# Optimization experiments

Measured on AMD Instinct MI355X. Metric: run time of the kernel, lower is better.

The kernel has to match this reference:

```python
import jax, jax.numpy as jnp
import numpy as np
from jax import lax

CONF_T = 0.5
IOU_T = 0.5
STRIDE = 8.0
NA = 3            # anchors per cell
NO = 16           # x,y,w,h,obj,10 landmarks,cls
G = 80            # grid size for 640/8
K = 300           # max detections kept into NMS
ANCHORS = np.array([[4., 5.], [8., 10.], [13., 16.]], dtype=np.float32)


def _conv(x, w, b, stride):
    y = lax.conv_general_dilated(x, w, (stride, stride), 'SAME',
                                 dimension_numbers=('NCHW', 'OIHW', 'NCHW'))
    return jax.nn.silu(y + b[None, :, None, None])


def _nms_single(boxes, scores):
    # boxes [N,4] xyxy, scores [N] (0 where below conf threshold)
    top_scores, idx = lax.top_k(scores, K)
    b = boxes[idx]                                   # [K,4]
    x1, y1, x2, y2 = b[:, 0], b[:, 1], b[:, 2], b[:, 3]
    area = jnp.maximum(x2 - x1, 0.) * jnp.maximum(y2 - y1, 0.)
    ix1 = jnp.maximum(x1[:, None], x1[None, :])
    iy1 = jnp.maximum(y1[:, None], y1[None, :])
    ix2 = jnp.minimum(x2[:, None], x2[None, :])
    iy2 = jnp.minimum(y2[:, None], y2[None, :])
    inter = jnp.maximum(ix2 - ix1, 0.) * jnp.maximum(iy2 - iy1, 0.)
    iou = inter / (area[:, None] + area[None, :] - inter + 1e-7)   # [K,K]

    ar = jnp.arange(K)

    def body(i, keep):
        sup = keep[i] & (iou[i] > IOU_T) & (ar > i)
        return keep & ~sup

    keep = lax.fori_loop(0, K, body, jnp.ones((K,), bool))
    keep = keep & (top_scores > 0.)
    return jnp.concatenate(
        [b, top_scores[:, None], keep.astype(b.dtype)[:, None]], axis=-1)  # [K,6]


def setup_inputs() -> dict:
    key = jax.random.key(0)
    ks = jax.random.split(key, 9)
    s = 0.1
    return {
        'x':  jax.random.uniform(ks[0], (16, 3, 640, 640), jnp.float32),
        'W1': jax.random.normal(ks[1], (16, 3, 3, 3), jnp.float32) * s,
        'b1': jnp.zeros((16,), jnp.float32),
        'W2': jax.random.normal(ks[2], (32, 16, 3, 3), jnp.float32) * s,
        'b2': jnp.zeros((32,), jnp.float32),
        'W3': jax.random.normal(ks[3], (64, 32, 3, 3), jnp.float32) * s,
        'b3': jnp.zeros((64,), jnp.float32),
        'Wh': jax.random.normal(ks[4], (NA * NO, 64, 1, 1), jnp.float32) * s,
        'bh': jnp.zeros((NA * NO,), jnp.float32),
    }


def reference(x, W1, b1, W2, b2, W3, b3, Wh, bh):
    B = x.shape[0]
    # backbone: stride-8 conv stem (YOLOv5n-like)
    f = _conv(x, W1, b1, 2)      # [B,16,320,320]
    f = _conv(f, W2, b2, 2)      # [B,32,160,160]
    f = _conv(f, W3, b3, 2)      # [B,64,80,80]
    h = lax.conv_general_dilated(f, Wh, (1, 1), 'SAME',
                                 dimension_numbers=('NCHW', 'OIHW', 'NCHW'))
    h = h + bh[None, :, None, None]                  # [B,NA*NO,G,G]
    p = h.reshape(B, NA, NO, G, G).transpose(0, 1, 3, 4, 2)  # [B,NA,G,G,NO]
    p = jax.nn.sigmoid(p)

    gy, gx = jnp.meshgrid(jnp.arange(G, dtype=jnp.float32),
                          jnp.arange(G, dtype=jnp.float32), indexing='ij')
    grid = jnp.stack([gx, gy], axis=-1)              # [G,G,2]
    anchors = jnp.asarray(ANCHORS)

    xy = (p[..., 0:2] * 2. - 0.5 + grid[None, None]) * STRIDE
    wh = (p[..., 2:4] * 2.) ** 2 * anchors[None, :, None, None, :]
    score = p[..., 4] * p[..., 15]                   # obj * cls

    boxes = jnp.concatenate([xy - wh / 2., xy + wh / 2.], axis=-1)
    boxes = boxes.reshape(B, -1, 4)                  # [B,N,4]
    score = score.reshape(B, -1)                     # [B,N]
    score = jnp.where(score > CONF_T, score, 0.)

    return jax.vmap(_nms_single)(boxes, score)       # [B,K,6]
```

## Files before the change

kernel.cpp:

```cpp
#include <hip/hip_runtime.h>
#include <math.h>

#define BATCH 16
#define GRID  80
#define NANCH 3
#define KTOP  300
#define NBOX  (NANCH*GRID*GRID)
#define SORT_CAP 8192

__device__ __forceinline__ float sigmoidf_(float x){ return 1.0f/(1.0f+expf(-x)); }

template<int CIN,int COUT,int C,int ICCH,int HIN,int HOUT,int TX,int TY,int MINW>
__global__ __launch_bounds__(256, MINW) void conv3x3s2_v7(
    const float* __restrict__ in, const float* __restrict__ w,
    const float* __restrict__ bias, float* __restrict__ out)
{
  constexpr int NTX = TX/4, NTY = TY/2, NSP = NTX*NTY, OCG = COUT/C;
  static_assert(NSP*OCG == 256, "bad thread layout");
  static_assert(C==4 || C==8, "C must be 4 or 8");
  constexpr int HR = 2*TY+1, HC = 2*TX+1;
  constexpr int NB4  = HC/4;
  constexpr int PADC = ((HC+3)/4)*4 + 4;
  constexpr int ILDSC = HR*PADC;
  constexpr int TBX = HOUT/TX, TBY = HOUT/TY;
  static_assert(TBX*TX == HOUT && TBY*TY == HOUT, "no masking");
  constexpr int NCH  = CIN/ICCH;
  constexpr int NH4  = ICCH*HR*NB4;
  constexpr int NH1  = ICCH*HR;
  constexpr int NWT  = ICCH*9*COUT;
  constexpr int NLD4 = (NH4+255)/256;
  constexpr int NLD1 = (NH1+255)/256;
  constexpr int NLDW = (NWT+255)/256;
  __shared__ float ilds[2][ICCH*ILDSC];
  __shared__ float wlds[2][NWT];

  const int t  = threadIdx.x;
  const int sx = t % NTX;
  const int sy = (t / NTX) % NTY;
  const int og = t / NSP;
  int blk = blockIdx.x;
  const int bx = blk % TBX; blk /= TBX;
  const int by = blk % TBY; blk /= TBY;
  const int b  = blk;

  const int ix0 = bx*2*TX, iy0 = by*2*TY;
  const int ylim = (iy0 + HR <= HIN) ? HR : (HIN - iy0);
  const bool tail_ok = (ix0 + NB4*4 < HIN);

  float4 hreg[NLD4];
  float  treg[NLD1];
  float  wreg[NLDW];

  auto load_regs = [&](int c0){
    #pragma unroll
    for (int l=0;l<NLD4;++l){
      int i = t + 256*l;
      float4 v = make_float4(0.f,0.f,0.f,0.f);
      if (i < NH4){
        int c = i/(HR*NB4), rm = i - c*(HR*NB4);
        int r = rm/NB4, m = rm - r*NB4;
        if (r < ylim)
          v = *(const float4*)(in + (size_t)(b*CIN + c0 + c)*HIN*HIN
                                  + (size_t)(iy0+r)*HIN + ix0 + 4*m);
      }
      hreg[l] = v;
    }
    #pragma unroll
    for (int l=0;l<NLD1;++l){
      int i = t + 256*l;
      float v = 0.f;
      if (i < NH1){
        int c = i/HR, r = i - c*HR;
        if (r < ylim && tail_ok)
          v = in[(size_t)(b*CIN + c0 + c)*HIN*HIN + (size_t)(iy0+r)*HIN + ix0 + NB4*4];
      }
      treg[l] = v;
    }
    #pragma unroll
    for (int l=0;l<NLDW;++l){
      int i = t + 256*l;
      float v = 0.f;
      if (i < NWT){
        int oc  = i % COUT;
        int k   = (i / COUT) % 9;
        int icl = i / (9*COUT);
        v = w[((size_t)oc*CIN + c0+icl)*9 + k];
      }
      wreg[l] = v;
    }
  };

  auto write_lds = [&](int bufi){
    #pragma unroll
    for (int l=0;l<NLD4;++l){
      int i = t + 256*l;
      if (i < NH4){
        int c = i/(HR*NB4), rm = i - c*(HR*NB4);
        int r = rm/NB4, m = rm - r*NB4;
        *(float4*)(&ilds[bufi][c*ILDSC + r*PADC + 4*((r>>2)&1) + 4*m]) = hreg[l];
      }
    }
    #pragma unroll
    for (int l=0;l<NLD1;++l){
      int i = t + 256*l;
      if (i < NH1){
        int c = i/HR, r = i - c*HR;
        ilds[bufi][c*ILDSC + r*PADC + 4*((r>>2)&1) + NB4*4] = treg[l];
      }
    }
    #pragma unroll
    for (int l=0;l<NLDW;++l){
      int i = t + 256*l;
      if (i < NWT) wlds[bufi][i] = wreg[l];
    }
  };

  float acc[C][2][4];
  #pragma unroll
  for (int j=0;j<C;++j){
    float bv = bias[og*C+j];
    #pragma unroll
    for (int py=0;py<2;++py)
      #pragma unroll
      for (int px=0;px<4;++px) acc[j][py][px]=bv;
  }

  load_regs(0);
  write_lds(0);
  __syncthreads();

  #pragma unroll 1
  for (int ch=0; ch<NCH; ++ch){
    const int cur = ch & 1;
    if (ch+1 < NCH) load_regs((ch+1)*ICCH);

    #pragma unroll 1
    for (int icl=0; icl<ICCH; ++icl){
      const float* wpb = &wlds[cur][icl*9*COUT] + og*C;
      float4 wk0[9], wk1[9];
      #pragma unroll
      for (int k=0;k<9;++k){
        wk0[k] = *(const float4*)(wpb + k*COUT);
        if constexpr (C==8) wk1[k] = *(const float4*)(wpb + k*COUT + 4);
      }
      const float* ipb = &ilds[cur][icl*ILDSC] + 8*sx;
      float rw[5][12];
      #pragma unroll
      for (int r=0;r<5;++r){
        const int rr = 4*sy + r;
        const float* rp = ipb + rr*PADC + 4*((rr>>2)&1);
        #pragma unroll
        for (int m=0;m<3;++m){
          float4 v4 = *(const float4*)(rp + 4*m);
          rw[r][4*m+0]=v4.x; rw[r][4*m+1]=v4.y; rw[r][4*m+2]=v4.z; rw[r][4*m+3]=v4.w;
        }
      }
      #pragma unroll
      for (int py=0;py<2;++py)
        #pragma unroll
        for (int ky=0;ky<3;++ky)
          #pragma unroll
          for (int kx=0;kx<3;++kx){
            const float4 wa = wk0[ky*3+kx];
            #pragma unroll
            for (int px=0;px<4;++px){
              const float xv = rw[2*py+ky][2*px+kx];
              acc[0][py][px] += xv*wa.x; acc[1][py][px] += xv*wa.y;
              acc[2][py][px] += xv*wa.z; acc[3][py][px] += xv*wa.w;
            }
            if constexpr (C==8){
              const float4 wb = wk1[ky*3+kx];
              #pragma unroll
              for (int px=0;px<4;++px){
                const float xv = rw[2*py+ky][2*px+kx];
                acc[4][py][px] += xv*wb.x; acc[5][py][px] += xv*wb.y;
                acc[6][py][px] += xv*wb.z; acc[7][py][px] += xv*wb.w;
              }
            }
          }
    }

    if (ch+1 < NCH) write_lds((ch+1)&1);
    __syncthreads();
  }

  const int oxb = bx*TX + sx*4;
  #pragma unroll
  for (int j=0;j<C;++j){
    int oc = og*C+j;
    #pragma unroll
    for (int py=0;py<2;++py){
      int oy = by*TY + sy*2 + py;
      float4 o4;
      float z0=acc[j][py][0], z1=acc[j][py][1], z2=acc[j][py][2], z3=acc[j][py][3];
      o4.x = z0/(1.0f+expf(-z0));
      o4.y = z1/(1.0f+expf(-z1));
      o4.z = z2/(1.0f+expf(-z2));
      o4.w = z3/(1.0f+expf(-z3));
      *(float4*)(out + ((size_t)(b*COUT+oc)*HOUT + oy)*HOUT + oxb) = o4;
    }
  }
}

__global__ __launch_bounds__(256, 1) void conv2_v12(
    const float* __restrict__ in, const float* __restrict__ w,
    const float* __restrict__ bias, float* __restrict__ out)
{
  constexpr int CIN=16, COUT=32, HIN=320, HOUT=160, TX=32, TY=16;
  constexpr int NTX=8, NTY=8;
  constexpr int C=8;
  constexpr int HR=2*TY+1;
  constexpr int NB4=(2*TX+1)/4;
  constexpr int PADC=72;
  constexpr int ILDSC=HR*PADC;
  constexpr int TBX=HOUT/TX, TBY=HOUT/TY;
  constexpr int NH4=HR*NB4;
  constexpr int NH1=HR;
  constexpr int NLD4=(NH4+255)/256;
  __shared__ float ilds[2][ILDSC];

  const int t  = threadIdx.x;
  const int sx = t % NTX;
  const int sy = (t / NTX) % NTY;
  const int og = t / 64;
  const int ocb = __builtin_amdgcn_readfirstlane(og * C);

  int blk = blockIdx.x;
  const int bx = blk % TBX; blk /= TBX;
  const int by = blk % TBY; blk /= TBY;
  const int b  = blk;

  const int ix0 = bx*2*TX, iy0 = by*2*TY;
  const int ylim = (iy0 + HR <= HIN) ? HR : (HIN - iy0);
  const bool tail_ok = (ix0 + NB4*4 < HIN);

  float4 hreg[NLD4];
  float  treg;

  auto load_regs = [&](int c0){
    #pragma unroll
    for (int l=0;l<NLD4;++l){
      int i = t + 256*l;
      float4 v = make_float4(0.f,0.f,0.f,0.f);
      if (i < NH4){
        int r = i/NB4, m = i - r*NB4;
        if (r < ylim)
          v = *(const float4*)(in + (size_t)(b*CIN + c0)*HIN*HIN
                                  + (size_t)(iy0+r)*HIN + ix0 + 4*m);
      }
      hreg[l] = v;
    }
    {
      float v = 0.f;
      if (t < NH1){
        int r = t;
        if (r < ylim && tail_ok)
          v = in[(size_t)(b*CIN + c0)*HIN*HIN + (size_t)(iy0+r)*HIN + ix0 + NB4*4];
      }
      treg = v;
    }
  };

  auto write_lds = [&](int bufi){
    #pragma unroll
    for (int l=0;l<NLD4;++l){
      int i = t + 256*l;
      if (i < NH4){
        int r = i/NB4, m = i - r*NB4;
        *(float4*)(&ilds[bufi][r*PADC + 4*((r>>2)&1) + 4*m]) = hreg[l];
      }
    }
    if (t < NH1){
      int r = t;
      ilds[bufi][r*PADC + 4*((r>>2)&1) + NB4*4] = treg;
    }
  };

  float acc[C][2][4];
  #pragma unroll
  for (int j=0;j<C;++j){
    float bv = bias[og*C+j];
    #pragma unroll
    for (int py=0;py<2;++py)
      #pragma unroll
      for (int px=0;px<4;++px) acc[j][py][px]=bv;
  }

  load_regs(0);
  write_lds(0);
  __syncthreads();

  #pragma unroll 1
  for (int ch=0; ch<CIN; ++ch){
    const int cur = ch & 1;
    if (ch+1 < CIN) load_regs(ch+1);

    const float* wg = w + ((size_t)ocb*CIN + ch)*9;
    const float* ipb = &ilds[cur][0] + 8*sx;

    #pragma unroll
    for (int ky=0;ky<3;++ky){
      float wv[3][8];
      #pragma unroll
      for (int j=0;j<8;++j){
        #pragma unroll
        for (int kx=0;kx<3;++kx)
          wv[kx][j] = wg[(size_t)j*(CIN*9) + ky*3 + kx];
      }
      {
        float ra[12];
        const int rr0 = 4*sy + ky;
        const float* rp0 = ipb + rr0*PADC + 4*((rr0>>2)&1);
        #pragma unroll
        for (int m=0;m<3;++m){
          float4 v0 = *(const float4*)(rp0 + 4*m);
          ra[4*m+0]=v0.x; ra[4*m+1]=v0.y; ra[4*m+2]=v0.z; ra[4*m+3]=v0.w;
        }
        #pragma unroll
        for (int kx=0;kx<3;++kx){
          #pragma unroll
          for (int px=0;px<4;++px){
            const float xv = ra[2*px+kx];
            acc[0][0][px] += xv*wv[kx][0]; acc[1][0][px] += xv*wv[kx][1];
            acc[2][0][px] += xv*wv[kx][2]; acc[3][0][px] += xv*wv[kx][3];
            acc[4][0][px] += xv*wv[kx][4]; acc[5][0][px] += xv*wv[kx][5];
            acc[6][0][px] += xv*wv[kx][6]; acc[7][0][px] += xv*wv[kx][7];
          }
        }
      }
      {
        float rb[12];
        const int rr1 = 4*sy + ky + 2;
        const float* rp1 = ipb + rr1*PADC + 4*((rr1>>2)&1);
        #pragma unroll
        for (int m=0;m<3;++m){
          float4 v1 = *(const float4*)(rp1 + 4*m);
          rb[4*m+0]=v1.x; rb[4*m+1]=v1.y; rb[4*m+2]=v1.z; rb[4*m+3]=v1.w;
        }
        #pragma unroll
        for (int kx=0;kx<3;++kx){
          #pragma unroll
          for (int px=0;px<4;++px){
            const float xv = rb[2*px+kx];
            acc[0][1][px] += xv*wv[kx][0]; acc[1][1][px] += xv*wv[kx][1];
            acc[2][1][px] += xv*wv[kx][2]; acc[3][1][px] += xv*wv[kx][3];
            acc[4][1][px] += xv*wv[kx][4]; acc[5][1][px] += xv*wv[kx][5];
            acc[6][1][px] += xv*wv[kx][6]; acc[7][1][px] += xv*wv[kx][7];
          }
        }
      }
    }

    if (ch+1 < CIN) write_lds((ch+1)&1);
    __syncthreads();
  }

  const int oxb = bx*TX + sx*4;
  #pragma unroll
  for (int j=0;j<C;++j){
    int oc = og*C+j;
    #pragma unroll
    for (int py=0;py<2;++py){
      int oy = by*TY + sy*2 + py;
      float4 o4;
      float z0=acc[j][py][0], z1=acc[j][py][1], z2=acc[j][py][2], z3=acc[j][py][3];
      o4.x = z0/(1.0f+expf(-z0));
      o4.y = z1/(1.0f+expf(-z1));
      o4.z = z2/(1.0f+expf(-z2));
      o4.w = z3/(1.0f+expf(-z3));
      *(float4*)(out + ((size_t)(b*COUT+oc)*HOUT + oy)*HOUT + oxb) = o4;
    }
  }
}

__global__ __launch_bounds__(256, 1) void conv3_decode_fused(
    const float* __restrict__ in,
    const float* __restrict__ w,
    const float* __restrict__ bias,
    const float* __restrict__ wh,
    const float* __restrict__ bh,
    float* __restrict__ boxes, float* __restrict__ scores)
{
  constexpr int CIN=32, COUT=64, C=8, ICCH=4, HIN=160, TX=16, TY=8;
  constexpr int NTX=4, NTY=8;
  constexpr int HR=2*TY+1, HC=2*TX+1;
  constexpr int NB4=HC/4;
  constexpr int PADC=((HC+3)/4)*4+4;
  constexpr int ILDSC=HR*PADC;
  constexpr int TBX=5, TBY=10;
  constexpr int NCH=CIN/ICCH;
  constexpr int NH4=ICCH*HR*NB4;
  constexpr int NH1=ICCH*HR;
  constexpr int NWT=ICCH*9*COUT;
  constexpr int NLD4=(NH4+255)/256, NLD1=(NH1+255)/256, NLDW=(NWT+255)/256;
  constexpr int F3S=69;
  __shared__ float smem[10048];
  float* ildsb = smem;
  float* wldsb = smem + 5440;
  float* f3l   = smem;

  const int t  = threadIdx.x;
  const int sp = t & 31;
  const int sx = sp & 3;
  const int sy = sp >> 2;
  const int og = t >> 5;
  int blk = blockIdx.x;
  const int bx = blk % TBX; blk /= TBX;
  const int by = blk % TBY; blk /= TBY;
  const int b  = blk;

  const int ix0 = bx*2*TX, iy0 = by*2*TY;
  const int ylim = (iy0 + HR <= HIN) ? HR : (HIN - iy0);
  const bool tail_ok = (ix0 + NB4*4 < HIN);

  float4 hreg[NLD4];
  float  treg[NLD1];
  float  wreg[NLDW];

  auto load_regs = [&](int c0){
    #pragma unroll
    for (int l=0;l<NLD4;++l){
      int i = t + 256*l;
      float4 v = make_float4(0.f,0.f,0.f,0.f);
      if (i < NH4){
        int c = i/(HR*NB4), rm = i - c*(HR*NB4);
        int r = rm/NB4, m = rm - r*NB4;
        if (r < ylim)
          v = *(const float4*)(in + (size_t)(b*CIN + c0 + c)*HIN*HIN
                                  + (size_t)(iy0+r)*HIN + ix0 + 4*m);
      }
      hreg[l] = v;
    }
    #pragma unroll
    for (int l=0;l<NLD1;++l){
      int i = t + 256*l;
      float v = 0.f;
      if (i < NH1){
        int c = i/HR, r = i - c*HR;
        if (r < ylim && tail_ok)
          v = in[(size_t)(b*CIN + c0 + c)*HIN*HIN + (size_t)(iy0+r)*HIN + ix0 + NB4*4];
      }
      treg[l] = v;
    }
    #pragma unroll
    for (int l=0;l<NLDW;++l){
      int i = t + 256*l;
      float v = 0.f;
      if (i < NWT){
        int oc  = i % COUT;
        int k   = (i / COUT) % 9;
        int icl = i / (9*COUT);
        v = w[((size_t)oc*CIN + c0+icl)*9 + k];
      }
      wreg[l] = v;
    }
  };

  auto write_lds = [&](int bufi){
    #pragma unroll
    for (int l=0;l<NLD4;++l){
      int i = t + 256*l;
      if (i < NH4){
        int c = i/(HR*NB4), rm = i - c*(HR*NB4);
        int r = rm/NB4, m = rm - r*NB4;
        *(float4*)(&ildsb[bufi*(ICCH*ILDSC) + c*ILDSC + r*PADC + 4*((r>>2)&1) + 4*m]) = hreg[l];
      }
    }
    #pragma unroll
    for (int l=0;l<NLD1;++l){
      int i = t + 256*l;
      if (i < NH1){
        int c = i/HR, r = i - c*HR;
        ildsb[bufi*(ICCH*ILDSC) + c*ILDSC + r*PADC + 4*((r>>2)&1) + NB4*4] = treg[l];
      }
    }
    #pragma unroll
    for (int l=0;l<NLDW;++l){
      int i = t + 256*l;
      if (i < NWT) wldsb[bufi*NWT + i] = wreg[l];
    }
  };

  float acc[C][4];
  #pragma unroll
  for (int j=0;j<C;++j){
    float bv = bias[og*C+j];
    #pragma unroll
    for (int px=0;px<4;++px) acc[j][px]=bv;
  }

  load_regs(0);
  write_lds(0);
  __syncthreads();

  #pragma unroll 1
  for (int ch=0; ch<NCH; ++ch){
    const int cur = ch & 1;
    if (ch+1 < NCH) load_regs((ch+1)*ICCH);

    #pragma unroll 1
    for (int icl=0; icl<ICCH; ++icl){
      const float* wpb = &wldsb[cur*NWT + icl*9*COUT] + og*C;
      const float* ipb = &ildsb[cur*(ICCH*ILDSC) + icl*ILDSC] + 8*sx;
      #pragma unroll
      for (int ky=0;ky<3;++ky){
        float row[12];
        {
          const int rr = 2*sy + ky;
          const float* rp = ipb + rr*PADC + 4*((rr>>2)&1);
          #pragma unroll
          for (int m=0;m<3;++m){
            float4 v4 = *(const float4*)(rp + 4*m);
            row[4*m+0]=v4.x; row[4*m+1]=v4.y; row[4*m+2]=v4.z; row[4*m+3]=v4.w;
          }
        }
        #pragma unroll
        for (int kx=0;kx<3;++kx){
          const float4 wa = *(const float4*)(wpb + (ky*3+kx)*COUT);
          const float4 wb = *(const float4*)(wpb + (ky*3+kx)*COUT + 4);
          #pragma unroll
          for (int px=0;px<4;++px){
            const float xv = row[2*px+kx];
            acc[0][px] += xv*wa.x; acc[1][px] += xv*wa.y;
            acc[2][px] += xv*wa.z; acc[3][px] += xv*wa.w;
            acc[4][px] += xv*wb.x; acc[5][px] += xv*wb.y;
            acc[6][px] += xv*wb.z; acc[7][px] += xv*wb.w;
          }
        }
      }
    }

    if (ch+1 < NCH) write_lds((ch+1)&1);
    __syncthreads();
  }

  #pragma unroll
  for (int j=0;j<C;++j){
    int oc = og*C+j;
    #pragma unroll
    for (int px=0;px<4;++px){
      int pxidx = sy*16 + sx*4+px;
      float z = acc[j][px];
      f3l[pxidx*F3S + oc] = z/(1.0f+expf(-z));
    }
  }
  __syncthreads();

  const float awv[3] = {4.0f, 8.0f, 13.0f};
  const float ahv[3] = {5.0f, 10.0f, 16.0f};
  const int chs[6] = {0,1,2,3,4,15};
  for (int q=t; q<384; q+=256){
    int p = q & 127;
    const int ua = __builtin_amdgcn_readfirstlane(q >> 7);
    float ac[6];
    #pragma unroll
    for (int j=0;j<6;++j) ac[j] = bh[ua*16 + chs[j]];
    const float* fp = f3l + p*F3S;
    const float* wp = wh + (size_t)ua*16*64;
    #pragma unroll 4
    for (int ic=0; ic<64; ic+=4){
      float4 fv = *(const float4*)(fp + ic);
      #pragma unroll
      for (int j=0;j<6;++j){
        float4 wv = *(const float4*)(wp + chs[j]*64 + ic);
        ac[j] += fv.x*wv.x; ac[j] += fv.y*wv.y;
        ac[j] += fv.z*wv.z; ac[j] += fv.w*wv.w;
      }
    }
    float p0 = sigmoidf_(ac[0]);
    float p1 = sigmoidf_(ac[1]);
    float p2 = sigmoidf_(ac[2]);
    float p3 = sigmoidf_(ac[3]);
    float p4 = sigmoidf_(ac[4]);
    float p15= sigmoidf_(ac[5]);
    int gx = bx*16 + (p & 15), gy = by*8 + (p >> 4);
    float cx = (p0*2.0f - 0.5f + (float)gx)*8.0f;
    float cy = (p1*2.0f - 0.5f + (float)gy)*8.0f;
    float ww = p2*2.0f; ww = ww*ww*awv[ua];
    float hh = p3*2.0f; hh = hh*hh*ahv[ua];
    float sc = p4*p15;
    sc = (sc > 0.5f) ? sc : 0.0f;
    int bi = ua*GRID*GRID + gy*GRID + gx;
    float* bo = boxes + ((size_t)b*NBOX + bi)*4;
    bo[0] = cx - ww*0.5f;
    bo[1] = cy - hh*0.5f;
    bo[2] = cx + ww*0.5f;
    bo[3] = cy + hh*0.5f;
    scores[(size_t)b*NBOX + bi] = sc;
  }
}

__global__ __launch_bounds__(1024) void topk_kernel(
    const float* __restrict__ boxes, const float* __restrict__ scores,
    float* __restrict__ nmsbuf, int* __restrict__ mcnt)
{
  __shared__ unsigned long long keys[SORT_CAP];
  __shared__ int   cntM;
  __shared__ int   sel[KTOP];
  __shared__ float selsc[KTOP];
  __shared__ int   wsum[16];
  __shared__ float rs[16];
  __shared__ int   ri[16];
  __shared__ unsigned clm[(NBOX+31)/32];

  const int b = blockIdx.x;
  const int t = threadIdx.x;
  const int lane = t & 63, wv = t >> 6;
  const float* scp = scores + (size_t)b*NBOX;

  if (t == 0) cntM = 0;
  __syncthreads();

  for (int i=t; i<NBOX; i+=1024){
    float v = scp[i];
    if (v > 0.0f){
      int p = atomicAdd(&cntM, 1);
      if (p < SORT_CAP)
        keys[p] = ((unsigned long long)__float_as_uint(v) << 32)
                | (unsigned)(0xFFFFFFFFu - (unsigned)i);
    }
  }
  __syncthreads();
  const int M = cntM;
  if (t == 0) mcnt[b] = M;

  if (M <= SORT_CAP){
    int P = 64; while (P < M) P <<= 1;
    for (int i=t; i<P; i+=1024) if (i >= M) keys[i] = 0ULL;
    __syncthreads();
    for (int k=2; k<=P; k<<=1){
      for (int j=k>>1; j>0; j>>=1){
        for (int i=t; i<P; i+=1024){
          int ixj = i ^ j;
          if (ixj > i){
            unsigned long long a = keys[i], c = keys[ixj];
            bool up = ((i & k) == 0);
            if (up ? (a < c) : (a > c)){ keys[i] = c; keys[ixj] = a; }
          }
        }
        __syncthreads();
      }
    }
    const int top = (M < KTOP) ? M : KTOP;
    if (t < top){
      unsigned long long kk = keys[t];
      selsc[t] = __uint_as_float((unsigned)(kk >> 32));
      sel[t]   = (int)(0xFFFFFFFFu - (unsigned)(kk & 0xFFFFFFFFu));
    }
    if (M < KTOP){
      const int need = KTOP - M;
      const int Cc = (NBOX + 1023)/1024;
      int lo = t*Cc, hi = lo+Cc; if (hi > NBOX) hi = NBOX; if (lo > NBOX) lo = NBOX;
      int zc = 0;
      for (int i=lo;i<hi;i++) if (scp[i] <= 0.0f) zc++;
      int v = zc;
      #pragma unroll
      for (int off=1; off<64; off<<=1){
        int n = __shfl_up(v, off);
        if (lane >= off) v += n;
      }
      if (lane == 63) wsum[wv] = v;
      __syncthreads();
      if (t == 0){
        int a = 0;
        for (int w=0; w<16; w++){ int tmp = wsum[w]; wsum[w] = a; a += tmp; }
      }
      __syncthreads();
      int r = wsum[wv] + v - zc;
      for (int i=lo;i<hi;i++){
        if (scp[i] <= 0.0f){
          if (r < need){ sel[M+r] = i; selsc[M+r] = 0.0f; }
          r++;
        }
      }
    }
    __syncthreads();
  } else {
    for (int i=t; i<(NBOX+31)/32; i+=1024) clm[i] = 0u;
    __syncthreads();
    for (int k=0;k<KTOP;k++){
      float best = -2.0f; int bi = NBOX;
      for (int i=t;i<NBOX;i+=1024){
        if (!((clm[i>>5] >> (i&31)) & 1u)){
          float v = scp[i];
          if (v > best){ best=v; bi=i; }
        }
      }
      #pragma unroll
      for (int off=32; off>0; off>>=1){
        float ov = __shfl_down(best, off);
        int   oi = __shfl_down(bi,   off);
        if (ov > best || (ov == best && oi < bi)){ best=ov; bi=oi; }
      }
      if (lane == 0){ rs[wv]=best; ri[wv]=bi; }
      __syncthreads();
      if (t == 0){
        for (int w=1; w<16; w++)
          if (rs[w] > best || (rs[w] == best && ri[w] < bi)){ best=rs[w]; bi=ri[w]; }
        sel[k]=bi; selsc[k]=best; clm[bi>>5] |= (1u << (bi&31));
      }
      __syncthreads();
    }
  }

  if (t < KTOP){
    const float* bp = boxes + ((size_t)b*NBOX + sel[t])*4;
    float x1=bp[0], y1=bp[1], x2=bp[2], y2=bp[3];
    float* o = nmsbuf + ((size_t)b*KTOP + t)*6;
    o[0]=x1; o[1]=y1; o[2]=x2; o[3]=y2;
    o[4]=selsc[t];
    o[5]=fmaxf(x2-x1,0.0f)*fmaxf(y2-y1,0.0f);
  }
}

__global__ __launch_bounds__(64, 1) void nms_kernel(
    const float* __restrict__ nmsbuf, const int* __restrict__ mcnt,
    float* __restrict__ out)
{
  const int b = blockIdx.x;
  const int lane = threadIdx.x;
  int Mtop = mcnt[b]; if (Mtop > KTOP) Mtop = KTOP;
  float X1[5],Y1[5],X2[5],Y2[5],AR[5],SC[5];
  unsigned keepm = 0;
  #pragma unroll
  for (int s5=0; s5<5; ++s5){
    int j = lane + 64*s5;
    if (j < KTOP){
      const float* p = nmsbuf + ((size_t)b*KTOP + j)*6;
      X1[s5]=p[0]; Y1[s5]=p[1]; X2[s5]=p[2]; Y2[s5]=p[3];
      SC[s5]=p[4]; AR[s5]=p[5];
      keepm |= (1u << s5);
    } else { X1[s5]=0;Y1[s5]=0;X2[s5]=0;Y2[s5]=0;AR[s5]=0;SC[s5]=0; }
  }
  for (int i=0;i<Mtop;i++){
    const int iw = i & 63, is = i >> 6;
    unsigned km = __shfl(keepm, iw);
    if ((km >> is) & 1u){
      float sx1 = (is==0)?X1[0]:(is==1)?X1[1]:(is==2)?X1[2]:(is==3)?X1[3]:X1[4];
      float sy1 = (is==0)?Y1[0]:(is==1)?Y1[1]:(is==2)?Y1[2]:(is==3)?Y1[3]:Y1[4];
      float sx2 = (is==0)?X2[0]:(is==1)?X2[1]:(is==2)?X2[2]:(is==3)?X2[3]:X2[4];
      float sy2 = (is==0)?Y2[0]:(is==1)?Y2[1]:(is==2)?Y2[2]:(is==3)?Y2[3]:Y2[4];
      float sa  = (is==0)?AR[0]:(is==1)?AR[1]:(is==2)?AR[2]:(is==3)?AR[3]:AR[4];
      float bx1=__shfl(sx1,iw), by1=__shfl(sy1,iw);
      float bx2=__shfl(sx2,iw), by2=__shfl(sy2,iw);
      float ba =__shfl(sa ,iw);
      #pragma unroll
      for (int s5=0; s5<5; ++s5){
        int j = lane + 64*s5;
        if (((keepm >> s5) & 1u) && j > i){
          float ix1=fmaxf(bx1,X1[s5]);
          float iy1=fmaxf(by1,Y1[s5]);
          float ix2=fminf(bx2,X2[s5]);
          float iy2=fminf(by2,Y2[s5]);
          float inter=fmaxf(ix2-ix1,0.0f)*fmaxf(iy2-iy1,0.0f);
          float iou = inter/(ba+AR[s5]-inter+1e-7f);
          if (iou > 0.5f) keepm &= ~(1u << s5);
        }
      }
    }
  }
  #pragma unroll
  for (int s5=0; s5<5; ++s5){
    int j = lane + 64*s5;
    if (j < KTOP){
      float scv = SC[s5];
      float kf  = (((keepm >> s5) & 1u) && scv > 0.0f) ? 1.0f : 0.0f;
      float* o = out + ((size_t)b*KTOP + j)*6;
      o[0]=X1[s5]; o[1]=Y1[s5]; o[2]=X2[s5]; o[3]=Y2[s5];
      o[4]=scv; o[5]=kf;
    }
  }
}

extern "C" void kernel_launch(void* const* d_in, const int* in_sizes, int n_in,
                              void* d_out, int out_size, void* d_ws, size_t ws_size,
                              hipStream_t stream) {
  const float* x  = (const float*)d_in[0];
  const float* W1 = (const float*)d_in[1];
  const float* b1 = (const float*)d_in[2];
  const float* W2 = (const float*)d_in[3];
  const float* b2 = (const float*)d_in[4];
  const float* W3 = (const float*)d_in[5];
  const float* b3 = (const float*)d_in[6];
  const float* Wh = (const float*)d_in[7];
  const float* bh = (const float*)d_in[8];
  float* out = (float*)d_out;
  float* ws  = (float*)d_ws;

  float* f1     = ws;
  float* f2     = ws + 26214400;
  float* boxes  = ws;
  float* scores = boxes + 1228800;
  float* nmsbuf = scores + 307200;
  int*   mcnt   = (int*)(nmsbuf + 28800);

  conv3x3s2_v7<3,16,8,1,640,320,64,16,1><<<5*20*BATCH, 256, 0, stream>>>(x,  W1, b1, f1);
  conv2_v12<<<5*10*BATCH, 256, 0, stream>>>(f1, W2, b2, f2);
  conv3_decode_fused<<<5*10*BATCH, 256, 0, stream>>>(f2, W3, b3, Wh, bh, boxes, scores);

  topk_kernel<<<BATCH, 1024, 0, stream>>>(boxes, scores, nmsbuf, mcnt);
  nms_kernel<<<BATCH, 64, 0, stream>>>(nmsbuf, mcnt, out);
}
```

Before: 362.6 us.

## Read conv3 weights as wave-uniform scalar loads instead of staging through LDS

The fused conv3+decode kernel no longer stages weights in shared memory. Each wave now owns 16 output channels, so weight addresses are wave-uniform and can be fetched with scalar loads straight from global memory. The thread layout moves from 8 channels x 4 pixels to 16 channels x 2 pixels, which shrinks LDS use and removes the weight loads and LDS writes from the double-buffer pipeline. The trade-off is more scalar memory traffic inside the inner loop, which is no longer prefetched, and less input reuse per LDS read.

```diff
diff --git a/kernel.cpp b/kernel.cpp
--- a/kernel.cpp
+++ b/kernel.cpp
@@ -381,8 +381,7 @@
     const float* __restrict__ bh,
     float* __restrict__ boxes, float* __restrict__ scores)
 {
-  constexpr int CIN=32, COUT=64, C=8, ICCH=4, HIN=160, TX=16, TY=8;
-  constexpr int NTX=4, NTY=8;
+  constexpr int CIN=32, COUT=64, C=16, ICCH=4, HIN=160, TX=16, TY=8;
   constexpr int HR=2*TY+1, HC=2*TX+1;
   constexpr int NB4=HC/4;
   constexpr int PADC=((HC+3)/4)*4+4;
@@ -391,19 +390,18 @@
   constexpr int NCH=CIN/ICCH;
   constexpr int NH4=ICCH*HR*NB4;
   constexpr int NH1=ICCH*HR;
-  constexpr int NWT=ICCH*9*COUT;
-  constexpr int NLD4=(NH4+255)/256, NLD1=(NH1+255)/256, NLDW=(NWT+255)/256;
+  constexpr int NLD4=(NH4+255)/256, NLD1=(NH1+255)/256;
   constexpr int F3S=69;
-  __shared__ float smem[10048];
+  __shared__ float smem[8832];
   float* ildsb = smem;
-  float* wldsb = smem + 5440;
   float* f3l   = smem;
 
-  const int t  = threadIdx.x;
-  const int sp = t & 31;
-  const int sx = sp & 3;
-  const int sy = sp >> 2;
-  const int og = t >> 5;
+  const int t    = threadIdx.x;
+  const int lane = t & 63;
+  const int sx   = lane & 7;
+  const int sy   = lane >> 3;
+  const int og   = t >> 6;
+  const int ocb  = __builtin_amdgcn_readfirstlane(og * C);
   int blk = blockIdx.x;
   const int bx = blk % TBX; blk /= TBX;
   const int by = blk % TBY; blk /= TBY;
@@ -415,7 +413,6 @@
 
   float4 hreg[NLD4];
   float  treg[NLD1];
-  float  wreg[NLDW];
 
   auto load_regs = [&](int c0){
     #pragma unroll
@@ -442,18 +439,6 @@
       }
       treg[l] = v;
     }
-    #pragma unroll
-    for (int l=0;l<NLDW;++l){
-      int i = t + 256*l;
-      float v = 0.f;
-      if (i < NWT){
-        int oc  = i % COUT;
-        int k   = (i / COUT) % 9;
-        int icl = i / (9*COUT);
-        v = w[((size_t)oc*CIN + c0+icl)*9 + k];
-      }
-      wreg[l] = v;
-    }
   };
 
   auto write_lds = [&](int bufi){
@@ -474,19 +459,13 @@
         ildsb[bufi*(ICCH*ILDSC) + c*ILDSC + r*PADC + 4*((r>>2)&1) + NB4*4] = treg[l];
       }
     }
-    #pragma unroll
-    for (int l=0;l<NLDW;++l){
-      int i = t + 256*l;
-      if (i < NWT) wldsb[bufi*NWT + i] = wreg[l];
-    }
   };
 
-  float acc[C][4];
+  float acc[C][2];
   #pragma unroll
   for (int j=0;j<C;++j){
-    float bv = bias[og*C+j];
-    #pragma unroll
-    for (int px=0;px<4;++px) acc[j][px]=bv;
+    float bv = bias[ocb+j];
+    acc[j][0]=bv; acc[j][1]=bv;
   }
 
   load_regs(0);
@@ -500,31 +479,34 @@
 
     #pragma unroll 1
     for (int icl=0; icl<ICCH; ++icl){
-      const float* wpb = &wldsb[cur*NWT + icl*9*COUT] + og*C;
-      const float* ipb = &ildsb[cur*(ICCH*ILDSC) + icl*ILDSC] + 8*sx;
+      const int ic = ch*ICCH + icl;
+      const float* wg = w + ((size_t)ocb*CIN + ic)*9;
+      const float* ipb = &ildsb[cur*(ICCH*ILDSC) + icl*ILDSC] + 4*sx;
       #pragma unroll
       for (int ky=0;ky<3;++ky){
-        float row[12];
+        float wv[3][16];
+        #pragma unroll
+        for (int j=0;j<16;++j){
+          #pragma unroll
+          for (int kx=0;kx<3;++kx)
+            wv[kx][j] = wg[(size_t)j*(CIN*9) + ky*3 + kx];
+        }
+        float row[5];
         {
           const int rr = 2*sy + ky;
           const float* rp = ipb + rr*PADC + 4*((rr>>2)&1);
+          float4 v4 = *(const float4*)(rp);
+          row[0]=v4.x; row[1]=v4.y; row[2]=v4.z; row[3]=v4.w;
+          row[4]=rp[4];
+        }
+        #pragma unroll
+        for (int kx=0;kx<3;++kx){
           #pragma unroll
-          for (int m=0;m<3;++m){
-            float4 v4 = *(const float4*)(rp + 4*m);
-            row[4*m+0]=v4.x; row[4*m+1]=v4.y; row[4*m+2]=v4.z; row[4*m+3]=v4.w;
-          }
-        }
-        #pragma unroll
-        for (int kx=0;kx<3;++kx){
-          const float4 wa = *(const float4*)(wpb + (ky*3+kx)*COUT);
-          const float4 wb = *(const float4*)(wpb + (ky*3+kx)*COUT + 4);
-          #pragma unroll
-          for (int px=0;px<4;++px){
-            const float xv = row[2*px+kx];
-            acc[0][px] += xv*wa.x; acc[1][px] += xv*wa.y;
-            acc[2][px] += xv*wa.z; acc[3][px] += xv*wa.w;
-            acc[4][px] += xv*wb.x; acc[5][px] += xv*wb.y;
-            acc[6][px] += xv*wb.z; acc[7][px] += xv*wb.w;
+          for (int p=0;p<2;++p){
+            const float xv = row[2*p+kx];
+            #pragma unroll
+            for (int j=0;j<16;++j)
+              acc[j][p] += xv*wv[kx][j];
           }
         }
       }
@@ -536,11 +518,11 @@
 
   #pragma unroll
   for (int j=0;j<C;++j){
-    int oc = og*C+j;
-    #pragma unroll
-    for (int px=0;px<4;++px){
-      int pxidx = sy*16 + sx*4+px;
-      float z = acc[j][px];
+    int oc = ocb+j;
+    #pragma unroll
+    for (int p=0;p<2;++p){
+      int pxidx = sy*16 + 2*sx + p;
+      float z = acc[j][p];
       f3l[pxidx*F3S + oc] = z/(1.0f+expf(-z));
     }
   }
```

Measured after the change: 387.3 us. +6.8%, slower.
